# Kernel optimization log

Measured on AMD Instinct MI355X. Metric: run time of the kernel, lower is better.

The kernel has to match this reference:

```python
import jax, jax.numpy as jnp
import numpy as np

B, H, W, C = 32, 112, 112, 192
K = 7  # spatial attention conv kernel size


def setup_inputs() -> dict:
    key = jax.random.key(0)
    k1, k2 = jax.random.split(key)
    x = jax.random.normal(k1, (B, H, W, C), dtype=jnp.float32)
    # he_normal init for 7x7 conv with 2 input channels, 1 output channel (HWIO)
    fan_in = K * K * 2
    conv_w = jax.random.normal(k2, (K, K, 2, 1), dtype=jnp.float32) * jnp.sqrt(2.0 / fan_in)
    return {"x": x, "conv_w": conv_w}


def reference(x, conv_w):
    # channel-wise reductions: [B,H,W,1] each
    avg_out = jnp.mean(x, axis=-1, keepdims=True)
    max_out = jnp.max(x, axis=-1, keepdims=True)
    concat = jnp.concatenate([avg_out, max_out], axis=-1)  # [B,H,W,2]
    # 7x7 conv, stride 1, SAME padding, no bias -> [B,H,W,1]
    att = jax.lax.conv_general_dilated(
        concat, conv_w,
        window_strides=(1, 1), padding="SAME",
        dimension_numbers=("NHWC", "HWIO", "NHWC"),
    )
    att = jax.nn.sigmoid(att)
    return x * att  # broadcast multiply back onto full feature map
```

## Files before the change

### kernel.cpp

```cpp
#include <hip/hip_runtime.h>
#include <math.h>

#define B_ 32
#define H_ 112
#define W_ 112
#define C_ 192
#define C4 (C_/4)
#define R_ 8
#define TILES (H_/R_)
#define HALO 3
#define SR (R_ + 2*HALO)
#define SW (W_ + 2*HALO)
#define NT_ 512

typedef float nf4 __attribute__((ext_vector_type(4)));

__global__ __launch_bounds__(512) void fused_kernel(const float* __restrict__ x,
                                                    const float* __restrict__ w,
                                                    float* __restrict__ out) {
    __shared__ float2 sm[SR][SW];
    __shared__ float  sw[98];
    __shared__ float  satt[R_ * W_];

    const int tid = threadIdx.x;
    const int b   = blockIdx.x / TILES;
    const int t   = blockIdx.x - b * TILES;
    const int y0  = t * R_;

    if (tid < 98) sw[tid] = w[tid];
    for (int i = tid; i < SR * SW; i += NT_)
        ((float2*)sm)[i] = make_float2(0.0f, 0.0f);
    __syncthreads();

    const int lane  = tid & 63;
    const int sub   = lane & 15;
    const int pbase = (tid >> 6) * 4 + (lane >> 4);
    for (int r = 0; r < SR; ++r) {
        const int yy = y0 + r - HALO;
        if (yy < 0 || yy >= H_) continue;
        const float* xrow = x + (size_t)(b * H_ + yy) * W_ * C_;
        #pragma unroll
        for (int i = 0; i < 4; ++i) {
            const int pos = i * 32 + pbase;
            if (pos < W_) {
                const float4* xp = (const float4*)(xrow + (size_t)pos * C_);
                float4 v0 = xp[sub];
                float4 v1 = xp[sub + 16];
                float4 v2 = xp[sub + 32];
                float s = (v0.x + v0.y + v0.z + v0.w)
                        + (v1.x + v1.y + v1.z + v1.w)
                        + (v2.x + v2.y + v2.z + v2.w);
                float m0 = fmaxf(fmaxf(v0.x, v0.y), fmaxf(v0.z, v0.w));
                float m1 = fmaxf(fmaxf(v1.x, v1.y), fmaxf(v1.z, v1.w));
                float m2 = fmaxf(fmaxf(v2.x, v2.y), fmaxf(v2.z, v2.w));
                float m  = fmaxf(m0, fmaxf(m1, m2));
                #pragma unroll
                for (int off = 8; off > 0; off >>= 1) {
                    s += __shfl_xor(s, off);
                    m = fmaxf(m, __shfl_xor(m, off));
                }
                if (sub == 0)
                    sm[r][HALO + pos] = make_float2(s * (1.0f / (float)C_), m);
            }
        }
    }
    __syncthreads();

    for (int idx = tid; idx < R_ * W_; idx += NT_) {
        const int rr  = idx / W_;
        const int col = idx - rr * W_;
        float acc = 0.0f;
        #pragma unroll
        for (int ky = 0; ky < 7; ++ky) {
            #pragma unroll
            for (int kx = 0; kx < 7; ++kx) {
                float2 am = sm[rr + ky][col + kx];
                acc = fmaf(am.x, sw[(ky * 7 + kx) * 2 + 0], acc);
                acc = fmaf(am.y, sw[(ky * 7 + kx) * 2 + 1], acc);
            }
        }
        satt[idx] = 1.0f / (1.0f + __expf(-acc));
    }
    __syncthreads();

    const size_t base4 = (size_t)(b * H_ + y0) * W_ * C4;
    const nf4* xr   = (const nf4*)x + base4;
    nf4*       orow = (nf4*)out + base4;
    #pragma unroll 4
    for (int k = 0; k < (R_ * W_ * C4) / NT_; ++k) {
        const int f4 = tid + k * NT_;
        nf4 v = xr[f4];
        v = v * satt[f4 / C4];
        __builtin_nontemporal_store(v, &orow[f4]);
    }
}

extern "C" void kernel_launch(void* const* d_in, const int* in_sizes, int n_in,
                              void* d_out, int out_size, void* d_ws, size_t ws_size,
                              hipStream_t stream) {
    const float* x = (const float*)d_in[0];
    const float* w = (const float*)d_in[1];
    float* out = (float*)d_out;
    fused_kernel<<<B_ * TILES, NT_, 0, stream>>>(x, w, out);
}
```

Before: 179.8 us.

## Use 7-row tiles with 1024-thread blocks, flat pixel mapping, and XCD-aware block swizzle

```diff
diff --git a/kernel.cpp b/kernel.cpp
--- a/kernel.cpp
+++ b/kernel.cpp
@@ -6,53 +6,55 @@
 #define W_ 112
 #define C_ 192
 #define C4 (C_/4)
-#define R_ 8
-#define TILES (H_/R_)
+#define R_ 7
+#define TPI (H_/R_)
+#define NBLK (B_*TPI)
 #define HALO 3
 #define SR (R_ + 2*HALO)
 #define SW (W_ + 2*HALO)
-#define NT_ 512
+#define SWP 120
+#define NT_ 1024
 
 typedef float nf4 __attribute__((ext_vector_type(4)));
 
-__global__ __launch_bounds__(512) void fused_kernel(const float* __restrict__ x,
-                                                    const float* __restrict__ w,
-                                                    float* __restrict__ out) {
-    __shared__ float2 sm[SR][SW];
+__global__ __launch_bounds__(NT_, 8) void fused_kernel(const float* __restrict__ x,
+                                                       const float* __restrict__ w,
+                                                       float* __restrict__ out) {
+    __shared__ float2 sm[SR][SWP];
     __shared__ float  sw[98];
     __shared__ float  satt[R_ * W_];
 
     const int tid = threadIdx.x;
-    const int b   = blockIdx.x / TILES;
-    const int t   = blockIdx.x - b * TILES;
+    const int bid = ((int)blockIdx.x & 7) * (NBLK / 8) + ((int)blockIdx.x >> 3);
+    const int b   = bid / TPI;
+    const int t   = bid - b * TPI;
     const int y0  = t * R_;
 
     if (tid < 98) sw[tid] = w[tid];
-    for (int i = tid; i < SR * SW; i += NT_)
+    for (int i = tid; i < SR * SWP; i += NT_)
         ((float2*)sm)[i] = make_float2(0.0f, 0.0f);
     __syncthreads();
 
-    const int lane  = tid & 63;
-    const int sub   = lane & 15;
-    const int pbase = (tid >> 6) * 4 + (lane >> 4);
-    for (int r = 0; r < SR; ++r) {
-        const int yy = y0 + r - HALO;
-        if (yy < 0 || yy >= H_) continue;
-        const float* xrow = x + (size_t)(b * H_ + yy) * W_ * C_;
-        #pragma unroll
-        for (int i = 0; i < 4; ++i) {
-            const int pos = i * 32 + pbase;
-            if (pos < W_) {
-                const float4* xp = (const float4*)(xrow + (size_t)pos * C_);
-                float4 v0 = xp[sub];
-                float4 v1 = xp[sub + 16];
-                float4 v2 = xp[sub + 32];
-                float s = (v0.x + v0.y + v0.z + v0.w)
-                        + (v1.x + v1.y + v1.z + v1.w)
-                        + (v2.x + v2.y + v2.z + v2.w);
-                float m0 = fmaxf(fmaxf(v0.x, v0.y), fmaxf(v0.z, v0.w));
-                float m1 = fmaxf(fmaxf(v1.x, v1.y), fmaxf(v1.z, v1.w));
-                float m2 = fmaxf(fmaxf(v2.x, v2.y), fmaxf(v2.z, v2.w));
+    const int g   = tid >> 4;
+    const int sub = tid & 15;
+    const float* xbase = x + (size_t)(b * H_) * W_ * C_;
+    for (int j = 0; j < (SR * W_ + 63) / 64; ++j) {
+        const int ps = j * 64 + g;
+        if (ps < SR * W_) {
+            const int r  = ps / W_;
+            const int cl = ps - r * W_;
+            const int yy = y0 + r - HALO;
+            if (yy >= 0 && yy < H_) {
+                const nf4* xp = (const nf4*)(xbase + ((size_t)yy * W_ + cl) * C_);
+                nf4 a0 = xp[sub];
+                nf4 a1 = xp[sub + 16];
+                nf4 a2 = xp[sub + 32];
+                float s = ((a0[0]+a0[1]) + (a0[2]+a0[3]))
+                        + ((a1[0]+a1[1]) + (a1[2]+a1[3]))
+                        + ((a2[0]+a2[1]) + (a2[2]+a2[3]));
+                float m0 = fmaxf(fmaxf(a0[0], a0[1]), fmaxf(a0[2], a0[3]));
+                float m1 = fmaxf(fmaxf(a1[0], a1[1]), fmaxf(a1[2], a1[3]));
+                float m2 = fmaxf(fmaxf(a2[0], a2[1]), fmaxf(a2[2], a2[3]));
                 float m  = fmaxf(m0, fmaxf(m1, m2));
                 #pragma unroll
                 for (int off = 8; off > 0; off >>= 1) {
@@ -60,38 +62,36 @@
                     m = fmaxf(m, __shfl_xor(m, off));
                 }
                 if (sub == 0)
-                    sm[r][HALO + pos] = make_float2(s * (1.0f / (float)C_), m);
+                    sm[r][HALO + cl] = make_float2(s * (1.0f / (float)C_), m);
             }
         }
     }
     __syncthreads();
 
-    for (int idx = tid; idx < R_ * W_; idx += NT_) {
-        const int rr  = idx / W_;
-        const int col = idx - rr * W_;
+    if (tid < R_ * W_) {
+        const int r  = tid / W_;
+        const int cl = tid - r * W_;
         float acc = 0.0f;
         #pragma unroll
         for (int ky = 0; ky < 7; ++ky) {
             #pragma unroll
             for (int kx = 0; kx < 7; ++kx) {
-                float2 am = sm[rr + ky][col + kx];
+                float2 am = sm[r + ky][cl + kx];
                 acc = fmaf(am.x, sw[(ky * 7 + kx) * 2 + 0], acc);
                 acc = fmaf(am.y, sw[(ky * 7 + kx) * 2 + 1], acc);
             }
         }
-        satt[idx] = 1.0f / (1.0f + __expf(-acc));
+        satt[tid] = 1.0f / (1.0f + __expf(-acc));
     }
     __syncthreads();
 
     const size_t base4 = (size_t)(b * H_ + y0) * W_ * C4;
     const nf4* xr   = (const nf4*)x + base4;
     nf4*       orow = (nf4*)out + base4;
-    #pragma unroll 4
-    for (int k = 0; k < (R_ * W_ * C4) / NT_; ++k) {
-        const int f4 = tid + k * NT_;
-        nf4 v = xr[f4];
-        v = v * satt[f4 / C4];
-        __builtin_nontemporal_store(v, &orow[f4]);
+    for (int f = tid; f < R_ * W_ * C4; f += NT_) {
+        nf4 v = xr[f];
+        v = v * satt[f / C4];
+        __builtin_nontemporal_store(v, &orow[f]);
     }
 }
 
@@ -101,5 +101,5 @@
     const float* x = (const float*)d_in[0];
     const float* w = (const float*)d_in[1];
     float* out = (float*)d_out;
-    fused_kernel<<<B_ * TILES, NT_, 0, stream>>>(x, w, out);
+    fused_kernel<<<NBLK, NT_, 0, stream>>>(x, w, out);
 }
```

New measurement: 173.6 us. 1.04x faster.
